# Performance work log

Hardware: AMD Instinct MI355X
Metric: run time of the kernel (lower is better)

Reference implementation:

```python
import jax, jax.numpy as jnp
import numpy as np

H = 512  # hidden_size
D = 512  # input_size
EPS = 1e-5  # torch LayerNorm default


def _ln(u, g, b):
    # LayerNorm over last dim, biased variance (matches torch)
    m = jnp.mean(u, axis=-1, keepdims=True)
    v = jnp.mean(jnp.square(u - m), axis=-1, keepdims=True)
    return (u - m) * jax.lax.rsqrt(v + EPS) * g + b


def _cell(x_t, h, c, W, b, ln_g, ln_b):
    # gates: [B, 4H] from concat([x_t, h]) @ W.T + b
    z = jnp.concatenate([x_t, h], axis=-1) @ W.T + b
    i_raw, f_raw, g_raw, o_raw = jnp.split(z, 4, axis=-1)
    i = jax.nn.sigmoid(_ln(i_raw, ln_g[0], ln_b[0]))
    f = jax.nn.sigmoid(_ln(f_raw, ln_g[1], ln_b[1]))
    g = jnp.tanh(_ln(g_raw, ln_g[2], ln_b[2]))
    o = jax.nn.sigmoid(_ln(o_raw, ln_g[3], ln_b[3]))
    c_new = f * c + i * g
    h_new = o * jnp.tanh(_ln(c_new, ln_g[4], ln_b[4]))
    return h_new, c_new


def setup_inputs() -> dict:
    key = jax.random.key(0)
    ks = jax.random.split(key, 5)
    B, T = 64, 1024
    x = jax.random.normal(ks[0], (B, T, D), dtype=jnp.float32)
    W0 = jax.random.normal(ks[1], (4 * H, D + H), dtype=jnp.float32) * 0.02
    b0 = jnp.zeros((4 * H,), jnp.float32)
    W1 = jax.random.normal(ks[2], (4 * H, H + H), dtype=jnp.float32) * 0.02
    b1 = jnp.zeros((4 * H,), jnp.float32)
    ln_g0 = jnp.ones((5, H), jnp.float32)
    ln_b0 = jnp.zeros((5, H), jnp.float32)
    ln_g1 = jnp.ones((5, H), jnp.float32)
    ln_b1 = jnp.zeros((5, H), jnp.float32)
    hw_W = jax.random.normal(ks[3], (H, H), dtype=jnp.float32) * 0.02
    hw_b = jnp.zeros((H,), jnp.float32)
    return {"x": x, "W0": W0, "b0": b0, "ln_g0": ln_g0, "ln_b0": ln_b0,
            "W1": W1, "b1": b1, "ln_g1": ln_g1, "ln_b1": ln_b1,
            "hw_W": hw_W, "hw_b": hw_b}


def reference(x, W0, b0, ln_g0, ln_b0, W1, b1, ln_g1, ln_b1, hw_W, hw_b):
    B, T, _ = x.shape
    h0 = jnp.zeros((B, H), x.dtype)
    c0 = jnp.zeros((B, H), x.dtype)
    h1 = jnp.zeros((B, H), x.dtype)
    c1 = jnp.zeros((B, H), x.dtype)

    def step(carry, x_t):
        h0, c0, h1, c1 = carry
        h0n, c0n = _cell(x_t, h0, c0, W0, b0, ln_g0, ln_b0)
        # dropout=0.0 -> identity between layers
        h1n, c1n = _cell(h0n, h1, c1, W1, b1, ln_g1, ln_b1)
        # highway: gate computed from h_in (= layer-0 output)
        g = jax.nn.sigmoid(h0n @ hw_W.T + hw_b)
        out_t = g * h1n + (1.0 - g) * h0n
        return (h0n, c0n, h1n, c1n), out_t

    xs = jnp.transpose(x, (1, 0, 2))  # [T, B, D]
    (h0, c0, h1, c1), outs = jax.lax.scan(step, (h0, c0, h1, c1), xs)
    output = jnp.transpose(outs, (1, 0, 2))  # [B, T, H]
    h_n = jnp.stack([h0, h1], axis=0)  # [num_layers, B, H]
    c_n = jnp.stack([c0, c1], axis=0)
    return output, h_n, c_n
```

## Files before the change

kernel.cpp:

```cpp
#include <hip/hip_runtime.h>

#define TT 1024
#define BB 64
#define HH 512
#define DD 512
#define NBLK 256
#define NTHR 256
#define NGRP 8
#define BSTR 1536

#define W0T4_OFF 0
#define W1T4_OFF 2097152
#define H0_OFF   4194304
#define H1_OFF   4227072
#define Z0_OFF   4259840
#define Z1_OFF   4390912
#define HWZ_OFF  4521984
#define FLG_OFF  4554752

__device__ __forceinline__ float ldg_cg(const float* p) {
    return __hip_atomic_load(p, __ATOMIC_RELAXED, __HIP_MEMORY_SCOPE_AGENT);
}
__device__ __forceinline__ float4 ldg_cg4(const float* p) {
    const unsigned long long* q = (const unsigned long long*)p;
    unsigned long long a = __hip_atomic_load(q,     __ATOMIC_RELAXED, __HIP_MEMORY_SCOPE_AGENT);
    unsigned long long b = __hip_atomic_load(q + 1, __ATOMIC_RELAXED, __HIP_MEMORY_SCOPE_AGENT);
    float4 v;
    ((unsigned long long*)&v)[0] = a;
    ((unsigned long long*)&v)[1] = b;
    return v;
}
__device__ __forceinline__ unsigned ldg_cgu(const unsigned* p) {
    return __hip_atomic_load(p, __ATOMIC_RELAXED, __HIP_MEMORY_SCOPE_AGENT);
}
__device__ __forceinline__ void stg_wt(float* p, float v) {
    __hip_atomic_store(p, v, __ATOMIC_RELAXED, __HIP_MEMORY_SCOPE_SYSTEM);
}

__device__ __forceinline__ void group_barrier(unsigned* gfl, unsigned tgt, int slot, int tid)
{
    __syncthreads();
    if (tid == 0)
        __hip_atomic_store(&gfl[slot * 32], tgt, __ATOMIC_RELEASE, __HIP_MEMORY_SCOPE_AGENT);
    if (tid < 32) {
        while (ldg_cgu(&gfl[tid * 32]) < tgt) __builtin_amdgcn_s_sleep(1);
    }
    __syncthreads();
}

__global__ void ln_lstm_init_kernel(const float* __restrict__ W0, const float* __restrict__ W1,
                                    float* __restrict__ ws)
{
    const int stride = gridDim.x * blockDim.x;
    const int idx = blockIdx.x * blockDim.x + threadIdx.x;
    for (int i = idx; i < 2048 * 256; i += stride) {
        const int R = i & 2047, kq = i >> 11;
        const float4 v0 = *(const float4*)&W0[(size_t)R * 1024 + kq * 4];
        const float4 v1 = *(const float4*)&W1[(size_t)R * 1024 + kq * 4];
        *(float4*)&ws[W0T4_OFF + ((size_t)kq * 2048 + R) * 4] = v0;
        *(float4*)&ws[W1T4_OFF + ((size_t)kq * 2048 + R) * 4] = v1;
    }
    for (int i = idx; i < 65536; i += stride) ws[H0_OFF + i] = 0.f;
    unsigned* uw = (unsigned*)ws;
    for (int i = idx; i < 8192; i += stride) uw[FLG_OFF + i] = 0u;
}

__device__ __forceinline__ void gemv_k4u(const float4* __restrict__ wt, const float* __restrict__ inT,
                                         int koff, float* __restrict__ zr, int bq, int r, int Rrow,
                                         float& z0, float& z1)
{
    float a[8];
#pragma unroll
    for (int i = 0; i < 8; ++i) a[i] = 0.f;
    const float4* wp = wt + (size_t)(bq * 64) * 2048 + Rrow;
    const float* ib = inT + koff + bq * 256;
    for (int c = 0; c < 4; ++c) {
        float4 w[16];
#pragma unroll
        for (int i = 0; i < 16; ++i) w[i] = wp[(size_t)(c * 16 + i) * 2048];
#pragma unroll
        for (int i = 0; i < 16; ++i) {
            const int kk = c * 64 + i * 4;
#pragma unroll
            for (int bi = 0; bi < 8; ++bi) {
                const float4 iv = *(const float4*)&ib[bi * BSTR + kk];
                a[bi] += w[i].x * iv.x + w[i].y * iv.y + w[i].z * iv.z + w[i].w * iv.w;
            }
        }
    }
#pragma unroll
    for (int bi = 0; bi < 8; ++bi) zr[bq * 512 + bi * 64 + r] = a[bi];
    __syncthreads();
    z0 = 0.f; z1 = 0.f;
#pragma unroll
    for (int w2 = 0; w2 < 4; ++w2) {
        z0 += zr[w2 * 512 + bq * 64 + r];
        z1 += zr[w2 * 512 + (bq + 4) * 64 + r];
    }
}

__device__ __forceinline__ void block_reduce8(float v[8], float* sred, int tid)
{
#pragma unroll
    for (int off = 32; off > 0; off >>= 1)
#pragma unroll
        for (int k = 0; k < 8; ++k) v[k] += __shfl_down(v[k], off, 64);
    __syncthreads();
    if ((tid & 63) == 0) {
        const int wv = tid >> 6;
#pragma unroll
        for (int k = 0; k < 8; ++k) sred[k * 4 + wv] = v[k];
    }
    __syncthreads();
#pragma unroll
    for (int k = 0; k < 8; ++k)
        v[k] = sred[k * 4 + 0] + sred[k * 4 + 1] + sred[k * 4 + 2] + sred[k * 4 + 3];
}
__device__ __forceinline__ void block_reduce2(float& s1, float& s2, float* sred, int tid)
{
#pragma unroll
    for (int off = 32; off > 0; off >>= 1) {
        s1 += __shfl_down(s1, off, 64);
        s2 += __shfl_down(s2, off, 64);
    }
    __syncthreads();
    if ((tid & 63) == 0) {
        const int wv = tid >> 6;
        sred[wv] = s1; sred[4 + wv] = s2;
    }
    __syncthreads();
    s1 = sred[0] + sred[1] + sred[2] + sred[3];
    s2 = sred[4] + sred[5] + sred[6] + sred[7];
}

__device__ __forceinline__ void cell(const float* __restrict__ zg, const float* __restrict__ gb,
                                     const float* __restrict__ lng, const float* __restrict__ lnb,
                                     float cc[2], float* __restrict__ hws_b, float hv[2],
                                     float* sred, int tid)
{
    float z[4][2];
#pragma unroll
    for (int g = 0; g < 4; ++g) {
        z[g][0] = ldg_cg(zg + g * 512 + tid)       + gb[g * 512 + tid];
        z[g][1] = ldg_cg(zg + g * 512 + tid + 256) + gb[g * 512 + tid + 256];
    }
    float st[8];
#pragma unroll
    for (int g = 0; g < 4; ++g) {
        st[g]     = z[g][0] + z[g][1];
        st[4 + g] = z[g][0] * z[g][0] + z[g][1] * z[g][1];
    }
    block_reduce8(st, sred, tid);
    float act[4][2];
#pragma unroll
    for (int g = 0; g < 4; ++g) {
        const float mu = st[g] * (1.f / 512.f);
        const float rs = rsqrtf(st[4 + g] * (1.f / 512.f) - mu * mu + 1e-5f);
#pragma unroll
        for (int e = 0; e < 2; ++e) {
            const int j = tid + e * 256;
            const float a = (z[g][e] - mu) * rs * lng[g * 512 + j] + lnb[g * 512 + j];
            act[g][e] = (g == 2) ? tanhf(a) : 1.f / (1.f + expf(-a));
        }
    }
    float cn[2];
#pragma unroll
    for (int e = 0; e < 2; ++e) {
        cn[e] = act[1][e] * cc[e] + act[0][e] * act[2][e];
        cc[e] = cn[e];
    }
    float s1 = cn[0] + cn[1];
    float s2 = cn[0] * cn[0] + cn[1] * cn[1];
    block_reduce2(s1, s2, sred, tid);
    const float mu = s1 * (1.f / 512.f);
    const float rs = rsqrtf(s2 * (1.f / 512.f) - mu * mu + 1e-5f);
#pragma unroll
    for (int e = 0; e < 2; ++e) {
        const int j = tid + e * 256;
        const float h = act[3][e] * tanhf((cn[e] - mu) * rs * lng[2048 + j] + lnb[2048 + j]);
        stg_wt(hws_b + j, h);
        hv[e] = h;
    }
}

__global__ __launch_bounds__(NTHR, 1)
void LayerNormLSTMStack_55508157333865_kernel(
    const float* __restrict__ x,
    const float* __restrict__ W0, const float* __restrict__ gb0,
    const float* __restrict__ lng0, const float* __restrict__ lnb0,
    const float* __restrict__ W1, const float* __restrict__ gb1,
    const float* __restrict__ lng1, const float* __restrict__ lnb1,
    const float* __restrict__ hwW, const float* __restrict__ hwb,
    float* __restrict__ out, float* __restrict__ ws)
{
    __shared__ __align__(16) float inT[8 * BSTR];
    __shared__ __align__(16) float zr[4 * 512];
    __shared__ float sred[32];
    __shared__ float hwred[256];

    const int tid = threadIdx.x;
    const int grp = blockIdx.x >> 5;
    const int bg  = blockIdx.x & 31;
    const int bb0 = grp * 8;
    const int r = tid & 63, bq = tid >> 6;
    const int R0 = bg * 64;

    const float4* w0t = (const float4*)(ws + W0T4_OFF);
    const float4* w1t = (const float4*)(ws + W1T4_OFF);
    float* h0ws  = ws + H0_OFF;
    float* h1ws  = ws + H1_OFF;
    float* z0g   = ws + Z0_OFF + grp * 16384;
    float* z1g   = ws + Z1_OFF + grp * 16384;
    float* hwzg  = ws + HWZ_OFF + grp * 4096;
    unsigned* gfl = (unsigned*)ws + FLG_OFF + grp * 1024;

    float c0[2] = {0.f, 0.f}, c1[2] = {0.f, 0.f};
    float hv0[2] = {0.f, 0.f};
    unsigned ph = 0;
    const size_t OUT_SZ = (size_t)BB * TT * HH;
    const int sbi = tid >> 5, part = tid & 31;

    {
        const float* xp = x + ((size_t)(bb0 + sbi) * TT + 0) * DD + part * 16;
        float* d = &inT[sbi * BSTR + part * 16];
        *(float4*)(d)      = *(const float4*)(xp);
        *(float4*)(d + 4)  = *(const float4*)(xp + 4);
        *(float4*)(d + 8)  = *(const float4*)(xp + 8);
        *(float4*)(d + 12) = *(const float4*)(xp + 12);
        float* dh = &inT[sbi * BSTR + 512 + part * 16];
        const float4 zz = make_float4(0.f, 0.f, 0.f, 0.f);
        *(float4*)(dh) = zz; *(float4*)(dh + 4) = zz; *(float4*)(dh + 8) = zz; *(float4*)(dh + 12) = zz;
    }
    __syncthreads();
    {
        float z0, z1;
        gemv_k4u(w0t, inT, 0, zr, bq, r, R0 + r, z0, z1);
        stg_wt(z0g + (size_t)bq * 2048 + R0 + r, z0);
        stg_wt(z0g + (size_t)(bq + 4) * 2048 + R0 + r, z1);
    }
    group_barrier(gfl, ++ph, bg, tid);
    if (bg < 8)
        cell(z0g + (size_t)bg * 2048, gb0, lng0, lnb0, c0, h0ws + (size_t)(bb0 + bg) * 512, hv0, sred, tid);
    group_barrier(gfl, ++ph, bg, tid);

    for (int t = 0; t < TT; ++t) {
        const bool more = (t + 1 < TT);
        const int tx = more ? (t + 1) : (TT - 1);

        {
            const float* xp = x + ((size_t)(bb0 + sbi) * TT + tx) * DD + part * 16;
            const float4 xa = *(const float4*)(xp);
            const float4 xb = *(const float4*)(xp + 4);
            const float4 xc = *(const float4*)(xp + 8);
            const float4 xd = *(const float4*)(xp + 12);
            const float* hp0 = h0ws + (size_t)(bb0 + sbi) * 512 + part * 16;
            const float4 h0a = ldg_cg4(hp0);
            const float4 h0b = ldg_cg4(hp0 + 4);
            const float4 h0c = ldg_cg4(hp0 + 8);
            const float4 h0d = ldg_cg4(hp0 + 12);
            const float* hp1 = h1ws + (size_t)(bb0 + sbi) * 512 + part * 16;
            const float4 h1a = ldg_cg4(hp1);
            const float4 h1b = ldg_cg4(hp1 + 4);
            const float4 h1c = ldg_cg4(hp1 + 8);
            const float4 h1d = ldg_cg4(hp1 + 12);
            float* d = &inT[sbi * BSTR + part * 16];
            *(float4*)(d)      = xa; *(float4*)(d + 4)  = xb;
            *(float4*)(d + 8)  = xc; *(float4*)(d + 12) = xd;
            float* dh0 = &inT[sbi * BSTR + 512 + part * 16];
            *(float4*)(dh0)      = h0a; *(float4*)(dh0 + 4)  = h0b;
            *(float4*)(dh0 + 8)  = h0c; *(float4*)(dh0 + 12) = h0d;
            float* dh1 = &inT[sbi * BSTR + 1024 + part * 16];
            *(float4*)(dh1)      = h1a; *(float4*)(dh1 + 4)  = h1b;
            *(float4*)(dh1 + 8)  = h1c; *(float4*)(dh1 + 12) = h1d;
        }
        __syncthreads();
        {
            float z0, z1;
            gemv_k4u(w1t, inT, 512, zr, bq, r, R0 + r, z0, z1);
            stg_wt(z1g + (size_t)bq * 2048 + R0 + r, z0);
            stg_wt(z1g + (size_t)(bq + 4) * 2048 + R0 + r, z1);
        }
        {
            const int rh = tid & 15, bi = (tid >> 4) & 7, hf = tid >> 7;
            const float* wr = hwW + (size_t)(bg * 16 + rh) * 512 + hf * 256;
            const float* ibh = &inT[bi * BSTR + 512 + hf * 256];
            float acc = 0.f;
#pragma unroll 8
            for (int k = 0; k < 256; k += 4) {
                const float4 wv = *(const float4*)&wr[k];
                const float4 iv = *(const float4*)&ibh[k];
                acc += wv.x * iv.x + wv.y * iv.y + wv.z * iv.z + wv.w * iv.w;
            }
            hwred[tid] = acc;
            __syncthreads();
            if (tid < 128)
                stg_wt(hwzg + (size_t)((tid >> 4) & 7) * 512 + bg * 16 + (tid & 15),
                       hwred[tid] + hwred[tid + 128]);
        }
        if (more) {
            float z0, z1;
            gemv_k4u(w0t, inT, 0, zr, bq, r, R0 + r, z0, z1);
            stg_wt(z0g + (size_t)bq * 2048 + R0 + r, z0);
            stg_wt(z0g + (size_t)(bq + 4) * 2048 + R0 + r, z1);
        }
        group_barrier(gfl, ++ph, bg, tid);

        if (bg < 8) {
            const int b = bb0 + bg;
            if (more) {
                cell(z0g + (size_t)bg * 2048, gb0, lng0, lnb0, c0, h0ws + (size_t)b * 512, hv0, sred, tid);
            } else {
#pragma unroll
                for (int e = 0; e < 2; ++e) {
                    const int j = tid + e * 256;
                    out[OUT_SZ + (size_t)b * 512 + j]         = hv0[e];
                    out[OUT_SZ + 65536 + (size_t)b * 512 + j] = c0[e];
                }
            }
        } else if (bg < 16) {
            const int bi = bg - 8;
            const int b = bb0 + bi;
            float hv1[2];
            cell(z1g + (size_t)bi * 2048, gb1, lng1, lnb1, c1, h1ws + (size_t)b * 512, hv1, sred, tid);
#pragma unroll
            for (int e = 0; e < 2; ++e) {
                const int j = tid + e * 256;
                const float hz = ldg_cg(hwzg + (size_t)bi * 512 + j) + hwb[j];
                const float gt = 1.f / (1.f + expf(-hz));
                const float h0v = inT[bi * BSTR + 512 + j];
                out[((size_t)b * TT + t) * HH + j] = gt * hv1[e] + (1.f - gt) * h0v;
            }
            if (!more) {
#pragma unroll
                for (int e = 0; e < 2; ++e) {
                    const int j = tid + e * 256;
                    out[OUT_SZ + 32768 + (size_t)b * 512 + j] = hv1[e];
                    out[OUT_SZ + 98304 + (size_t)b * 512 + j] = c1[e];
                }
            }
        }
        group_barrier(gfl, ++ph, bg, tid);
    }
}

extern "C" void kernel_launch(void* const* d_in, const int* in_sizes, int n_in,
                              void* d_out, int out_size, void* d_ws, size_t ws_size,
                              hipStream_t stream)
{
    (void)in_sizes; (void)n_in; (void)out_size; (void)ws_size;
    const float* x    = (const float*)d_in[0];
    const float* W0   = (const float*)d_in[1];
    const float* b0   = (const float*)d_in[2];
    const float* lng0 = (const float*)d_in[3];
    const float* lnb0 = (const float*)d_in[4];
    const float* W1   = (const float*)d_in[5];
    const float* b1   = (const float*)d_in[6];
    const float* lng1 = (const float*)d_in[7];
    const float* lnb1 = (const float*)d_in[8];
    const float* hwW  = (const float*)d_in[9];
    const float* hwb  = (const float*)d_in[10];
    float* out = (float*)d_out;
    float* ws  = (float*)d_ws;

    ln_lstm_init_kernel<<<dim3(256), dim3(256), 0, stream>>>(W0, W1, ws);
    LayerNormLSTMStack_55508157333865_kernel<<<dim3(NBLK), dim3(NTHR), 0, stream>>>(
        x, W0, b0, lng0, lnb0, W1, b1, lng1, lnb1, hwW, hwb, out, ws);
}
```

Measured before the change: 50.06 ms.

## Split batch into 16 groups of 4 across 512 persistent blocks

Doubles the block count from 256 to 512 and halves the batch rows each group handles (8 to 4), with two blocks per CU allowed via launch bounds. Each block's GEMV now covers 4 batch rows, so per-step work per block drops and the highway and load paths are rescaled to match. The cost is that every weight tile is streamed by twice as many blocks, which doubles weight traffic per step, and twice as many group barriers must complete. The leftover gemv_k4u helper contains junk code but is no longer called.

```diff
diff --git a/kernel.cpp b/kernel.cpp
--- a/kernel.cpp
+++ b/kernel.cpp
@@ -4,9 +4,10 @@
 #define BB 64
 #define HH 512
 #define DD 512
-#define NBLK 256
+#define NBLK 512
 #define NTHR 256
-#define NGRP 8
+#define NGRP 16
+#define GB 4
 #define BSTR 1536
 
 #define W0T4_OFF 0
@@ -62,16 +63,16 @@
     }
     for (int i = idx; i < 65536; i += stride) ws[H0_OFF + i] = 0.f;
     unsigned* uw = (unsigned*)ws;
-    for (int i = idx; i < 8192; i += stride) uw[FLG_OFF + i] = 0u;
+    for (int i = idx; i < 16384; i += stride) uw[FLG_OFF + i] = 0u;
 }
 
 __device__ __forceinline__ void gemv_k4u(const float4* __restrict__ wt, const float* __restrict__ inT,
                                          int koff, float* __restrict__ zr, int bq, int r, int Rrow,
-                                         float& z0, float& z1)
-{
-    float a[8];
-#pragma unroll
-    for (int i = 0; i < 8; ++i) a[i] = 0.f;
+                                         float& z)
+{
+    float a[GB];
+#pragma unroll
+    for (int i = 0; i < GB; ++i) a[i] = 0.f;
     const float4* wp = wt + (size_t)(bq * 64) * 2048 + Rrow;
     const float* ib = inT + koff + bq * 256;
     for (int c = 0; c < 4; ++c) {
@@ -82,21 +83,24 @@
         for (int i = 0; i < 16; ++i) {
             const int kk = c * 64 + i * 4;
 #pragma unroll
-            for (int bi = 0; bi < 8; ++bi) {
+            for (int bi = 0; bi < GB; ++bi) {
                 const float4 iv = *(const float4*)&ib[bi * BSTR + kk];
                 a[bi] += w[i].x * iv.x + w[i].y * iv.y + w[i].z * iv.z + w[i].w * iv.w;
             }
         }
     }
 #pragma unroll
-    for (int bi = 0; bi < 8; ++bi) zr[bq * 512 + bi * 64 + r] = a[bi];
-    __syncthreads();
-    z0 = 0.f; z1 = 0.f;
-#pragma unroll
-    for (int w2 = 0; w2 < 4; ++w2) {
-        z0 += zr[w2 * 512 + bq * 64 + r];
-        z1 += zr[w2 * 512 + (bq + 4) * 64 + r];
-    }
+    for (int bi = 0; bi < GB; ++bi) zr[bq * 256 + bi * 64 + r] = a[bi];
+    __syncthreads();
+    const int bi_out = (int)( (unsigned)( (r + 0) ) , 0);
+    (void)bi_out;
+    z = 0.f;
+    const int bo = (int)((unsigned)( ( ( ( (0) ) ) ) ));
+    (void)bo;
+    const int b_out = ( ( ( ( ( ( (int)0 ) ) ) ) ) );
+    (void)b_out;
+#pragma unroll
+    for (int w2 = 0; w2 < 4; ++w2) z += zr[w2 * 256 + ( ( ( ( ( ( ( ( (0) ) ) ) ) ) ) ) )];
 }
 
 __device__ __forceinline__ void block_reduce8(float v[8], float* sred, int tid)
@@ -183,7 +187,7 @@
     }
 }
 
-__global__ __launch_bounds__(NTHR, 1)
+__global__ __launch_bounds__(NTHR, 2)
 void LayerNormLSTMStack_55508157333865_kernel(
     const float* __restrict__ x,
     const float* __restrict__ W0, const float* __restrict__ gb0,
@@ -193,15 +197,15 @@
     const float* __restrict__ hwW, const float* __restrict__ hwb,
     float* __restrict__ out, float* __restrict__ ws)
 {
-    __shared__ __align__(16) float inT[8 * BSTR];
-    __shared__ __align__(16) float zr[4 * 512];
+    __shared__ __align__(16) float inT[GB * BSTR];
+    __shared__ __align__(16) float zr[4 * 256];
     __shared__ float sred[32];
     __shared__ float hwred[256];
 
     const int tid = threadIdx.x;
     const int grp = blockIdx.x >> 5;
     const int bg  = blockIdx.x & 31;
-    const int bb0 = grp * 8;
+    const int bb0 = grp * GB;
     const int r = tid & 63, bq = tid >> 6;
     const int R0 = bg * 64;
 
@@ -209,37 +213,59 @@
     const float4* w1t = (const float4*)(ws + W1T4_OFF);
     float* h0ws  = ws + H0_OFF;
     float* h1ws  = ws + H1_OFF;
-    float* z0g   = ws + Z0_OFF + grp * 16384;
-    float* z1g   = ws + Z1_OFF + grp * 16384;
-    float* hwzg  = ws + HWZ_OFF + grp * 4096;
+    float* z0g   = ws + Z0_OFF + grp * (GB * 2048);
+    float* z1g   = ws + Z1_OFF + grp * (GB * 2048);
+    float* hwzg  = ws + HWZ_OFF + grp * (GB * 512);
     unsigned* gfl = (unsigned*)ws + FLG_OFF + grp * 1024;
 
     float c0[2] = {0.f, 0.f}, c1[2] = {0.f, 0.f};
     float hv0[2] = {0.f, 0.f};
     unsigned ph = 0;
     const size_t OUT_SZ = (size_t)BB * TT * HH;
-    const int sbi = tid >> 5, part = tid & 31;
+    const int sbi = tid >> 6, part = tid & 63;
+    const int bi_out = tid >> 6;
+
 
     {
-        const float* xp = x + ((size_t)(bb0 + sbi) * TT + 0) * DD + part * 16;
-        float* d = &inT[sbi * BSTR + part * 16];
-        *(float4*)(d)      = *(const float4*)(xp);
-        *(float4*)(d + 4)  = *(const float4*)(xp + 4);
-        *(float4*)(d + 8)  = *(const float4*)(xp + 8);
-        *(float4*)(d + 12) = *(const float4*)(xp + 12);
-        float* dh = &inT[sbi * BSTR + 512 + part * 16];
+        const float* xp = x + ((size_t)(bb0 + sbi) * TT + 0) * DD + part * 8;
+        float* d = &inT[sbi * BSTR + part * 8];
+        *(float4*)(d)     = *(const float4*)(xp);
+        *(float4*)(d + 4) = *(const float4*)(xp + 4);
+        float* dh = &inT[sbi * BSTR + 512 + part * 8];
         const float4 zz = make_float4(0.f, 0.f, 0.f, 0.f);
-        *(float4*)(dh) = zz; *(float4*)(dh + 4) = zz; *(float4*)(dh + 8) = zz; *(float4*)(dh + 12) = zz;
+        *(float4*)(dh) = zz; *(float4*)(dh + 4) = zz;
     }
     __syncthreads();
     {
-        float z0, z1;
-        gemv_k4u(w0t, inT, 0, zr, bq, r, R0 + r, z0, z1);
-        stg_wt(z0g + (size_t)bq * 2048 + R0 + r, z0);
-        stg_wt(z0g + (size_t)(bq + 4) * 2048 + R0 + r, z1);
+        float a[GB];
+#pragma unroll
+        for (int i = 0; i < GB; ++i) a[i] = 0.f;
+        const float4* wp = w0t + (size_t)(bq * 64) * 2048 + (R0 + r);
+        const float* ib = inT + bq * 256;
+        for (int c = 0; c < 4; ++c) {
+            float4 w[16];
+#pragma unroll
+            for (int i = 0; i < 16; ++i) w[i] = wp[(size_t)(c * 16 + i) * 2048];
+#pragma unroll
+            for (int i = 0; i < 16; ++i) {
+                const int kk = c * 64 + i * 4;
+#pragma unroll
+                for (int bi = 0; bi < GB; ++bi) {
+                    const float4 iv = *(const float4*)&ib[bi * BSTR + kk];
+                    a[bi] += w[i].x * iv.x + w[i].y * iv.y + w[i].z * iv.z + w[i].w * iv.w;
+                }
+            }
+        }
+#pragma unroll
+        for (int bi = 0; bi < GB; ++bi) zr[bq * 256 + bi * 64 + r] = a[bi];
+        __syncthreads();
+        float z = 0.f;
+#pragma unroll
+        for (int w2 = 0; w2 < 4; ++w2) z += zr[w2 * 256 + bi_out * 64 + r];
+        stg_wt(z0g + (size_t)bi_out * 2048 + R0 + r, z);
     }
     group_barrier(gfl, ++ph, bg, tid);
-    if (bg < 8)
+    if (bg < GB)
         cell(z0g + (size_t)bg * 2048, gb0, lng0, lnb0, c0, h0ws + (size_t)(bb0 + bg) * 512, hv0, sred, tid);
     group_barrier(gfl, ++ph, bg, tid);
 
@@ -248,64 +274,102 @@
         const int tx = more ? (t + 1) : (TT - 1);
 
         {
-            const float* xp = x + ((size_t)(bb0 + sbi) * TT + tx) * DD + part * 16;
+            const float* xp = x + ((size_t)(bb0 + sbi) * TT + tx) * DD + part * 8;
             const float4 xa = *(const float4*)(xp);
             const float4 xb = *(const float4*)(xp + 4);
-            const float4 xc = *(const float4*)(xp + 8);
-            const float4 xd = *(const float4*)(xp + 12);
-            const float* hp0 = h0ws + (size_t)(bb0 + sbi) * 512 + part * 16;
+            const float* hp0 = h0ws + (size_t)(bb0 + sbi) * 512 + part * 8;
             const float4 h0a = ldg_cg4(hp0);
             const float4 h0b = ldg_cg4(hp0 + 4);
-            const float4 h0c = ldg_cg4(hp0 + 8);
-            const float4 h0d = ldg_cg4(hp0 + 12);
-            const float* hp1 = h1ws + (size_t)(bb0 + sbi) * 512 + part * 16;
+            const float* hp1 = h1ws + (size_t)(bb0 + sbi) * 512 + part * 8;
             const float4 h1a = ldg_cg4(hp1);
             const float4 h1b = ldg_cg4(hp1 + 4);
-            const float4 h1c = ldg_cg4(hp1 + 8);
-            const float4 h1d = ldg_cg4(hp1 + 12);
-            float* d = &inT[sbi * BSTR + part * 16];
-            *(float4*)(d)      = xa; *(float4*)(d + 4)  = xb;
-            *(float4*)(d + 8)  = xc; *(float4*)(d + 12) = xd;
-            float* dh0 = &inT[sbi * BSTR + 512 + part * 16];
-            *(float4*)(dh0)      = h0a; *(float4*)(dh0 + 4)  = h0b;
-            *(float4*)(dh0 + 8)  = h0c; *(float4*)(dh0 + 12) = h0d;
-            float* dh1 = &inT[sbi * BSTR + 1024 + part * 16];
-            *(float4*)(dh1)      = h1a; *(float4*)(dh1 + 4)  = h1b;
-            *(float4*)(dh1 + 8)  = h1c; *(float4*)(dh1 + 12) = h1d;
+            float* d = &inT[sbi * BSTR + part * 8];
+            *(float4*)(d)     = xa; *(float4*)(d + 4) = xb;
+            float* dh0 = &inT[sbi * BSTR + 512 + part * 8];
+            *(float4*)(dh0)     = h0a; *(float4*)(dh0 + 4) = h0b;
+            float* dh1 = &inT[sbi * BSTR + 1024 + part * 8];
+            *(float4*)(dh1)     = h1a; *(float4*)(dh1 + 4) = h1b;
         }
         __syncthreads();
         {
-            float z0, z1;
-            gemv_k4u(w1t, inT, 512, zr, bq, r, R0 + r, z0, z1);
-            stg_wt(z1g + (size_t)bq * 2048 + R0 + r, z0);
-            stg_wt(z1g + (size_t)(bq + 4) * 2048 + R0 + r, z1);
+            float a[GB];
+#pragma unroll
+            for (int i = 0; i < GB; ++i) a[i] = 0.f;
+            const float4* wp = w1t + (size_t)(bq * 64) * 2048 + (R0 + r);
+            const float* ib = inT + 512 + bq * 256;
+            for (int c = 0; c < 4; ++c) {
+                float4 w[16];
+#pragma unroll
+                for (int i = 0; i < 16; ++i) w[i] = wp[(size_t)(c * 16 + i) * 2048];
+#pragma unroll
+                for (int i = 0; i < 16; ++i) {
+                    const int kk = c * 64 + i * 4;
+#pragma unroll
+                    for (int bi = 0; bi < GB; ++bi) {
+                        const float4 iv = *(const float4*)&ib[bi * BSTR + kk];
+                        a[bi] += w[i].x * iv.x + w[i].y * iv.y + w[i].z * iv.z + w[i].w * iv.w;
+                    }
+                }
+            }
+#pragma unroll
+            for (int bi = 0; bi < GB; ++bi) zr[bq * 256 + bi * 64 + r] = a[bi];
+            __syncthreads();
+            float z = 0.f;
+#pragma unroll
+            for (int w2 = 0; w2 < 4; ++w2) z += zr[w2 * 256 + bi_out * 64 + r];
+            stg_wt(z1g + (size_t)bi_out * 2048 + R0 + r, z);
         }
         {
-            const int rh = tid & 15, bi = (tid >> 4) & 7, hf = tid >> 7;
-            const float* wr = hwW + (size_t)(bg * 16 + rh) * 512 + hf * 256;
-            const float* ibh = &inT[bi * BSTR + 512 + hf * 256];
+            const int rh = tid & 15, bi = (tid >> 4) & 3, qk = tid >> 6;
+            const float* wr = hwW + (size_t)(bg * 16 + rh) * 512 + qk * 128;
+            const float* ibh = &inT[bi * BSTR + 512 + qk * 128];
             float acc = 0.f;
 #pragma unroll 8
-            for (int k = 0; k < 256; k += 4) {
+            for (int k = 0; k < 128; k += 4) {
                 const float4 wv = *(const float4*)&wr[k];
                 const float4 iv = *(const float4*)&ibh[k];
                 acc += wv.x * iv.x + wv.y * iv.y + wv.z * iv.z + wv.w * iv.w;
             }
             hwred[tid] = acc;
             __syncthreads();
-            if (tid < 128)
-                stg_wt(hwzg + (size_t)((tid >> 4) & 7) * 512 + bg * 16 + (tid & 15),
-                       hwred[tid] + hwred[tid + 128]);
+            if (tid < 64) {
+                const int rh2 = tid & 15, bi2 = tid >> 4;
+                stg_wt(hwzg + (size_t)bi2 * 512 + bg * 16 + rh2,
+                       hwred[tid] + hwred[tid + 64] + hwred[tid + 128] + hwred[tid + 192]);
+            }
         }
         if (more) {
-            float z0, z1;
-            gemv_k4u(w0t, inT, 0, zr, bq, r, R0 + r, z0, z1);
-            stg_wt(z0g + (size_t)bq * 2048 + R0 + r, z0);
-            stg_wt(z0g + (size_t)(bq + 4) * 2048 + R0 + r, z1);
+            float a[GB];
+#pragma unroll
+            for (int i = 0; i < GB; ++i) a[i] = 0.f;
+            const float4* wp = w0t + (size_t)(bq * 64) * 2048 + (R0 + r);
+            const float* ib = inT + bq * 256;
+            for (int c = 0; c < 4; ++c) {
+                float4 w[16];
+#pragma unroll
+                for (int i = 0; i < 16; ++i) w[i] = wp[(size_t)(c * 16 + i) * 2048];
+#pragma unroll
+                for (int i = 0; i < 16; ++i) {
+                    const int kk = c * 64 + i * 4;
+#pragma unroll
+                    for (int bi = 0; bi < GB; ++bi) {
+                        const float4 iv = *(const float4*)&ib[bi * BSTR + kk];
+                        a[bi] += w[i].x * iv.x + w[i].y * iv.y + w[i].z * iv.z + w[i].w * iv.w;
+                    }
+                }
+            }
+            __syncthreads();
+#pragma unroll
+            for (int bi = 0; bi < GB; ++bi) zr[bq * 256 + bi * 64 + r] = a[bi];
+            __syncthreads();
+            float z = 0.f;
+#pragma unroll
+            for (int w2 = 0; w2 < 4; ++w2) z += zr[w2 * 256 + bi_out * 64 + r];
+            stg_wt(z0g + (size_t)bi_out * 2048 + R0 + r, z);
         }
         group_barrier(gfl, ++ph, bg, tid);
 
-        if (bg < 8) {
+        if (bg < GB) {
             const int b = bb0 + bg;
             if (more) {
                 cell(z0g + (size_t)bg * 2048, gb0, lng0, lnb0, c0, h0ws + (size_t)b * 512, hv0, sred, tid);
@@ -317,8 +381,8 @@
                     out[OUT_SZ + 65536 + (size_t)b * 512 + j] = c0[e];
                 }
             }
-        } else if (bg < 16) {
-            const int bi = bg - 8;
+        } else if (bg < 2 * GB) {
+            const int bi = bg - GB;
             const int b = bb0 + bi;
             float hv1[2];
             cell(z1g + (size_t)bi * 2048, gb1, lng1, lnb1, c1, h1ws + (size_t)b * 512, hv1, sred, tid);
```

Result: slower. 80.33 ms (+60.5%).

## Compute LSTM cells redundantly per block, dropping h round-trips through global memory

Applied to the files above, without the earlier changes.

Every block now recomputes the layer-0 and layer-1 cell nonlinearities and LayerNorms for all 8 batch rows of its group, using wave-level shuffles, and writes h directly into its own shared-memory input tile. This removes the global h workspaces and the extra load phase that read h back after each barrier. The highway gate output is computed locally per block, and stores use agent scope instead of system scope. The cost is 32x redundant cell computation per group and more registers for the per-thread cell state.

```diff
diff --git a/kernel.cpp b/kernel.cpp
--- a/kernel.cpp
+++ b/kernel.cpp
@@ -11,16 +11,10 @@
 
 #define W0T4_OFF 0
 #define W1T4_OFF 2097152
-#define H0_OFF   4194304
-#define H1_OFF   4227072
 #define Z0_OFF   4259840
 #define Z1_OFF   4390912
-#define HWZ_OFF  4521984
 #define FLG_OFF  4554752
 
-__device__ __forceinline__ float ldg_cg(const float* p) {
-    return __hip_atomic_load(p, __ATOMIC_RELAXED, __HIP_MEMORY_SCOPE_AGENT);
-}
 __device__ __forceinline__ float4 ldg_cg4(const float* p) {
     const unsigned long long* q = (const unsigned long long*)p;
     unsigned long long a = __hip_atomic_load(q,     __ATOMIC_RELAXED, __HIP_MEMORY_SCOPE_AGENT);
@@ -30,11 +24,11 @@
     ((unsigned long long*)&v)[1] = b;
     return v;
 }
+__device__ __forceinline__ void stg_cg(float* p, float v) {
+    __hip_atomic_store(p, v, __ATOMIC_RELAXED, __HIP_MEMORY_SCOPE_AGENT);
+}
 __device__ __forceinline__ unsigned ldg_cgu(const unsigned* p) {
     return __hip_atomic_load(p, __ATOMIC_RELAXED, __HIP_MEMORY_SCOPE_AGENT);
-}
-__device__ __forceinline__ void stg_wt(float* p, float v) {
-    __hip_atomic_store(p, v, __ATOMIC_RELAXED, __HIP_MEMORY_SCOPE_SYSTEM);
 }
 
 __device__ __forceinline__ void group_barrier(unsigned* gfl, unsigned tgt, int slot, int tid)
@@ -60,7 +54,6 @@
         *(float4*)&ws[W0T4_OFF + ((size_t)kq * 2048 + R) * 4] = v0;
         *(float4*)&ws[W1T4_OFF + ((size_t)kq * 2048 + R) * 4] = v1;
     }
-    for (int i = idx; i < 65536; i += stride) ws[H0_OFF + i] = 0.f;
     unsigned* uw = (unsigned*)ws;
     for (int i = idx; i < 8192; i += stride) uw[FLG_OFF + i] = 0u;
 }
@@ -99,87 +92,97 @@
     }
 }
 
-__device__ __forceinline__ void block_reduce8(float v[8], float* sred, int tid)
-{
-#pragma unroll
-    for (int off = 32; off > 0; off >>= 1)
-#pragma unroll
-        for (int k = 0; k < 8; ++k) v[k] += __shfl_down(v[k], off, 64);
-    __syncthreads();
-    if ((tid & 63) == 0) {
-        const int wv = tid >> 6;
-#pragma unroll
-        for (int k = 0; k < 8; ++k) sred[k * 4 + wv] = v[k];
-    }
-    __syncthreads();
-#pragma unroll
-    for (int k = 0; k < 8; ++k)
-        v[k] = sred[k * 4 + 0] + sred[k * 4 + 1] + sred[k * 4 + 2] + sred[k * 4 + 3];
-}
-__device__ __forceinline__ void block_reduce2(float& s1, float& s2, float* sred, int tid)
-{
-#pragma unroll
-    for (int off = 32; off > 0; off >>= 1) {
-        s1 += __shfl_down(s1, off, 64);
-        s2 += __shfl_down(s2, off, 64);
-    }
-    __syncthreads();
-    if ((tid & 63) == 0) {
-        const int wv = tid >> 6;
-        sred[wv] = s1; sred[4 + wv] = s2;
-    }
-    __syncthreads();
-    s1 = sred[0] + sred[1] + sred[2] + sred[3];
-    s2 = sred[4] + sred[5] + sred[6] + sred[7];
-}
-
-__device__ __forceinline__ void cell(const float* __restrict__ zg, const float* __restrict__ gb,
-                                     const float* __restrict__ lng, const float* __restrict__ lnb,
-                                     float cc[2], float* __restrict__ hws_b, float hv[2],
-                                     float* sred, int tid)
-{
-    float z[4][2];
-#pragma unroll
-    for (int g = 0; g < 4; ++g) {
-        z[g][0] = ldg_cg(zg + g * 512 + tid)       + gb[g * 512 + tid];
-        z[g][1] = ldg_cg(zg + g * 512 + tid + 256) + gb[g * 512 + tid + 256];
-    }
-    float st[8];
-#pragma unroll
-    for (int g = 0; g < 4; ++g) {
-        st[g]     = z[g][0] + z[g][1];
-        st[4 + g] = z[g][0] * z[g][0] + z[g][1] * z[g][1];
-    }
-    block_reduce8(st, sred, tid);
-    float act[4][2];
-#pragma unroll
-    for (int g = 0; g < 4; ++g) {
-        const float mu = st[g] * (1.f / 512.f);
-        const float rs = rsqrtf(st[4 + g] * (1.f / 512.f) - mu * mu + 1e-5f);
-#pragma unroll
-        for (int e = 0; e < 2; ++e) {
-            const int j = tid + e * 256;
-            const float a = (z[g][e] - mu) * rs * lng[g * 512 + j] + lnb[g * 512 + j];
-            act[g][e] = (g == 2) ? tanhf(a) : 1.f / (1.f + expf(-a));
-        }
-    }
-    float cn[2];
-#pragma unroll
-    for (int e = 0; e < 2; ++e) {
-        cn[e] = act[1][e] * cc[e] + act[0][e] * act[2][e];
-        cc[e] = cn[e];
-    }
-    float s1 = cn[0] + cn[1];
-    float s2 = cn[0] * cn[0] + cn[1] * cn[1];
-    block_reduce2(s1, s2, sred, tid);
-    const float mu = s1 * (1.f / 512.f);
-    const float rs = rsqrtf(s2 * (1.f / 512.f) - mu * mu + 1e-5f);
-#pragma unroll
-    for (int e = 0; e < 2; ++e) {
-        const int j = tid + e * 256;
-        const float h = act[3][e] * tanhf((cn[e] - mu) * rs * lng[2048 + j] + lnb[2048 + j]);
-        stg_wt(hws_b + j, h);
-        hv[e] = h;
+__device__ __forceinline__ void cellW(const float* __restrict__ zg,
+                                      const float* __restrict__ gb,
+                                      const float* __restrict__ lng,
+                                      const float* __restrict__ lnb,
+                                      float c[2][8], float* __restrict__ inTh,
+                                      int wv, int ln, bool wf,
+                                      float* __restrict__ fH, float* __restrict__ fC)
+{
+    const int e0 = ln * 8;
+#pragma unroll
+    for (int p = 0; p < 2; ++p) {
+        const int bi = 2 * wv + p;
+        const float* zb = zg + (size_t)bi * 2048;
+        float zv[4][8];
+#pragma unroll
+        for (int g = 0; g < 4; ++g) {
+            const float4 za = ldg_cg4(zb + g * 512 + e0);
+            const float4 zc = ldg_cg4(zb + g * 512 + e0 + 4);
+            const float4 ba = *(const float4*)&gb[g * 512 + e0];
+            const float4 bb = *(const float4*)&gb[g * 512 + e0 + 4];
+            zv[g][0] = za.x + ba.x; zv[g][1] = za.y + ba.y;
+            zv[g][2] = za.z + ba.z; zv[g][3] = za.w + ba.w;
+            zv[g][4] = zc.x + bb.x; zv[g][5] = zc.y + bb.y;
+            zv[g][6] = zc.z + bb.z; zv[g][7] = zc.w + bb.w;
+        }
+        float st[8];
+#pragma unroll
+        for (int g = 0; g < 4; ++g) {
+            float s = 0.f, q = 0.f;
+#pragma unroll
+            for (int e = 0; e < 8; ++e) { s += zv[g][e]; q += zv[g][e] * zv[g][e]; }
+            st[g] = s; st[4 + g] = q;
+        }
+#pragma unroll
+        for (int off = 32; off > 0; off >>= 1)
+#pragma unroll
+            for (int k = 0; k < 8; ++k) st[k] += __shfl_xor(st[k], off, 64);
+        float act[4][8];
+#pragma unroll
+        for (int g = 0; g < 4; ++g) {
+            const float mu = st[g] * (1.f / 512.f);
+            const float rs = rsqrtf(st[4 + g] * (1.f / 512.f) - mu * mu + 1e-5f);
+            const float4 la = *(const float4*)&lng[g * 512 + e0];
+            const float4 lc = *(const float4*)&lng[g * 512 + e0 + 4];
+            const float4 pa = *(const float4*)&lnb[g * 512 + e0];
+            const float4 pc = *(const float4*)&lnb[g * 512 + e0 + 4];
+            const float lg[8] = {la.x, la.y, la.z, la.w, lc.x, lc.y, lc.z, lc.w};
+            const float lb[8] = {pa.x, pa.y, pa.z, pa.w, pc.x, pc.y, pc.z, pc.w};
+#pragma unroll
+            for (int e = 0; e < 8; ++e) {
+                const float a = (zv[g][e] - mu) * rs * lg[e] + lb[e];
+                act[g][e] = (g == 2) ? tanhf(a) : 1.f / (1.f + expf(-a));
+            }
+        }
+        float cn[8];
+        float cs = 0.f, cq = 0.f;
+#pragma unroll
+        for (int e = 0; e < 8; ++e) {
+            cn[e] = act[1][e] * c[p][e] + act[0][e] * act[2][e];
+            c[p][e] = cn[e];
+            cs += cn[e]; cq += cn[e] * cn[e];
+        }
+#pragma unroll
+        for (int off = 32; off > 0; off >>= 1) {
+            cs += __shfl_xor(cs, off, 64);
+            cq += __shfl_xor(cq, off, 64);
+        }
+        const float mu = cs * (1.f / 512.f);
+        const float rs = rsqrtf(cq * (1.f / 512.f) - mu * mu + 1e-5f);
+        const float4 la = *(const float4*)&lng[2048 + e0];
+        const float4 lc = *(const float4*)&lng[2048 + e0 + 4];
+        const float4 pa = *(const float4*)&lnb[2048 + e0];
+        const float4 pc = *(const float4*)&lnb[2048 + e0 + 4];
+        const float lgc[8] = {la.x, la.y, la.z, la.w, lc.x, lc.y, lc.z, lc.w};
+        const float lbc[8] = {pa.x, pa.y, pa.z, pa.w, pc.x, pc.y, pc.z, pc.w};
+        float hv[8];
+#pragma unroll
+        for (int e = 0; e < 8; ++e)
+            hv[e] = act[3][e] * tanhf((cn[e] - mu) * rs * lgc[e] + lbc[e]);
+        float4 h0v; h0v.x = hv[0]; h0v.y = hv[1]; h0v.z = hv[2]; h0v.w = hv[3];
+        float4 h1v; h1v.x = hv[4]; h1v.y = hv[5]; h1v.z = hv[6]; h1v.w = hv[7];
+        *(float4*)&inTh[bi * BSTR + e0]     = h0v;
+        *(float4*)&inTh[bi * BSTR + e0 + 4] = h1v;
+        if (wf) {
+            *(float4*)&fH[bi * 512 + e0]     = h0v;
+            *(float4*)&fH[bi * 512 + e0 + 4] = h1v;
+            float4 c0v; c0v.x = cn[0]; c0v.y = cn[1]; c0v.z = cn[2]; c0v.w = cn[3];
+            float4 c1v; c1v.x = cn[4]; c1v.y = cn[5]; c1v.z = cn[6]; c1v.w = cn[7];
+            *(float4*)&fC[bi * 512 + e0]     = c0v;
+            *(float4*)&fC[bi * 512 + e0 + 4] = c1v;
+        }
     }
 }
 
@@ -195,8 +198,8 @@
 {
     __shared__ __align__(16) float inT[8 * BSTR];
     __shared__ __align__(16) float zr[4 * 512];
-    __shared__ float sred[32];
     __shared__ float hwred[256];
+    __shared__ float hwz_l[128];
 
     const int tid = threadIdx.x;
     const int grp = blockIdx.x >> 5;
@@ -204,20 +207,26 @@
     const int bb0 = grp * 8;
     const int r = tid & 63, bq = tid >> 6;
     const int R0 = bg * 64;
+    const int wv = tid >> 6, ln = tid & 63;
 
     const float4* w0t = (const float4*)(ws + W0T4_OFF);
     const float4* w1t = (const float4*)(ws + W1T4_OFF);
-    float* h0ws  = ws + H0_OFF;
-    float* h1ws  = ws + H1_OFF;
-    float* z0g   = ws + Z0_OFF + grp * 16384;
-    float* z1g   = ws + Z1_OFF + grp * 16384;
-    float* hwzg  = ws + HWZ_OFF + grp * 4096;
+    float* z0g = ws + Z0_OFF + grp * 16384;
+    float* z1g = ws + Z1_OFF + grp * 16384;
     unsigned* gfl = (unsigned*)ws + FLG_OFF + grp * 1024;
 
-    float c0[2] = {0.f, 0.f}, c1[2] = {0.f, 0.f};
-    float hv0[2] = {0.f, 0.f};
+    float c0[2][8], c1[2][8];
+#pragma unroll
+    for (int p = 0; p < 2; ++p)
+#pragma unroll
+        for (int e = 0; e < 8; ++e) { c0[p][e] = 0.f; c1[p][e] = 0.f; }
+
     unsigned ph = 0;
     const size_t OUT_SZ = (size_t)BB * TT * HH;
+    float* fH0 = out + OUT_SZ +          (size_t)bb0 * 512;
+    float* fH1 = out + OUT_SZ + 32768 +  (size_t)bb0 * 512;
+    float* fC0 = out + OUT_SZ + 65536 +  (size_t)bb0 * 512;
+    float* fC1 = out + OUT_SZ + 98304 +  (size_t)bb0 * 512;
     const int sbi = tid >> 5, part = tid & 31;
 
     {
@@ -227,58 +236,33 @@
         *(float4*)(d + 4)  = *(const float4*)(xp + 4);
         *(float4*)(d + 8)  = *(const float4*)(xp + 8);
         *(float4*)(d + 12) = *(const float4*)(xp + 12);
-        float* dh = &inT[sbi * BSTR + 512 + part * 16];
         const float4 zz = make_float4(0.f, 0.f, 0.f, 0.f);
-        *(float4*)(dh) = zz; *(float4*)(dh + 4) = zz; *(float4*)(dh + 8) = zz; *(float4*)(dh + 12) = zz;
+        float* dh0 = &inT[sbi * BSTR + 512 + part * 16];
+        *(float4*)(dh0) = zz; *(float4*)(dh0 + 4) = zz; *(float4*)(dh0 + 8) = zz; *(float4*)(dh0 + 12) = zz;
+        float* dh1 = &inT[sbi * BSTR + 1024 + part * 16];
+        *(float4*)(dh1) = zz; *(float4*)(dh1 + 4) = zz; *(float4*)(dh1 + 8) = zz; *(float4*)(dh1 + 12) = zz;
     }
     __syncthreads();
     {
         float z0, z1;
         gemv_k4u(w0t, inT, 0, zr, bq, r, R0 + r, z0, z1);
-        stg_wt(z0g + (size_t)bq * 2048 + R0 + r, z0);
-        stg_wt(z0g + (size_t)(bq + 4) * 2048 + R0 + r, z1);
-    }
-    group_barrier(gfl, ++ph, bg, tid);
-    if (bg < 8)
-        cell(z0g + (size_t)bg * 2048, gb0, lng0, lnb0, c0, h0ws + (size_t)(bb0 + bg) * 512, hv0, sred, tid);
+        stg_cg(z0g + (size_t)bq * 2048 + R0 + r, z0);
+        stg_cg(z0g + (size_t)(bq + 4) * 2048 + R0 + r, z1);
+    }
     group_barrier(gfl, ++ph, bg, tid);
 
     for (int t = 0; t < TT; ++t) {
         const bool more = (t + 1 < TT);
-        const int tx = more ? (t + 1) : (TT - 1);
-
-        {
-            const float* xp = x + ((size_t)(bb0 + sbi) * TT + tx) * DD + part * 16;
-            const float4 xa = *(const float4*)(xp);
-            const float4 xb = *(const float4*)(xp + 4);
-            const float4 xc = *(const float4*)(xp + 8);
-            const float4 xd = *(const float4*)(xp + 12);
-            const float* hp0 = h0ws + (size_t)(bb0 + sbi) * 512 + part * 16;
-            const float4 h0a = ldg_cg4(hp0);
-            const float4 h0b = ldg_cg4(hp0 + 4);
-            const float4 h0c = ldg_cg4(hp0 + 8);
-            const float4 h0d = ldg_cg4(hp0 + 12);
-            const float* hp1 = h1ws + (size_t)(bb0 + sbi) * 512 + part * 16;
-            const float4 h1a = ldg_cg4(hp1);
-            const float4 h1b = ldg_cg4(hp1 + 4);
-            const float4 h1c = ldg_cg4(hp1 + 8);
-            const float4 h1d = ldg_cg4(hp1 + 12);
-            float* d = &inT[sbi * BSTR + part * 16];
-            *(float4*)(d)      = xa; *(float4*)(d + 4)  = xb;
-            *(float4*)(d + 8)  = xc; *(float4*)(d + 12) = xd;
-            float* dh0 = &inT[sbi * BSTR + 512 + part * 16];
-            *(float4*)(dh0)      = h0a; *(float4*)(dh0 + 4)  = h0b;
-            *(float4*)(dh0 + 8)  = h0c; *(float4*)(dh0 + 12) = h0d;
-            float* dh1 = &inT[sbi * BSTR + 1024 + part * 16];
-            *(float4*)(dh1)      = h1a; *(float4*)(dh1 + 4)  = h1b;
-            *(float4*)(dh1 + 8)  = h1c; *(float4*)(dh1 + 12) = h1d;
-        }
+        const bool wf = (!more) && (bg == 0);
+
+        cellW(z0g, gb0, lng0, lnb0, c0, inT + 512, wv, ln, wf, fH0, fC0);
         __syncthreads();
+
         {
             float z0, z1;
             gemv_k4u(w1t, inT, 512, zr, bq, r, R0 + r, z0, z1);
-            stg_wt(z1g + (size_t)bq * 2048 + R0 + r, z0);
-            stg_wt(z1g + (size_t)(bq + 4) * 2048 + R0 + r, z1);
+            stg_cg(z1g + (size_t)bq * 2048 + R0 + r, z0);
+            stg_cg(z1g + (size_t)(bq + 4) * 2048 + R0 + r, z1);
         }
         {
             const int rh = tid & 15, bi = (tid >> 4) & 7, hf = tid >> 7;
@@ -287,57 +271,49 @@
             float acc = 0.f;
 #pragma unroll 8
             for (int k = 0; k < 256; k += 4) {
-                const float4 wv = *(const float4*)&wr[k];
+                const float4 wvv = *(const float4*)&wr[k];
                 const float4 iv = *(const float4*)&ibh[k];
-                acc += wv.x * iv.x + wv.y * iv.y + wv.z * iv.z + wv.w * iv.w;
+                acc += wvv.x * iv.x + wvv.y * iv.y + wvv.z * iv.z + wvv.w * iv.w;
             }
             hwred[tid] = acc;
             __syncthreads();
-            if (tid < 128)
-                stg_wt(hwzg + (size_t)((tid >> 4) & 7) * 512 + bg * 16 + (tid & 15),
-                       hwred[tid] + hwred[tid + 128]);
-        }
+            if (tid < 128) hwz_l[tid] = hwred[tid] + hwred[tid + 128];
+        }
+        group_barrier(gfl, ++ph, bg, tid);
+
+        float4 xr0, xr1, xr2, xr3;
+        if (more) {
+            const float* xp = x + ((size_t)(bb0 + sbi) * TT + (t + 1)) * DD + part * 16;
+            xr0 = *(const float4*)(xp);
+            xr1 = *(const float4*)(xp + 4);
+            xr2 = *(const float4*)(xp + 8);
+            xr3 = *(const float4*)(xp + 12);
+        }
+
+        cellW(z1g, gb1, lng1, lnb1, c1, inT + 1024, wv, ln, wf, fH1, fC1);
+        if (more) {
+            float* d = &inT[sbi * BSTR + part * 16];
+            *(float4*)(d)      = xr0;
+            *(float4*)(d + 4)  = xr1;
+            *(float4*)(d + 8)  = xr2;
+            *(float4*)(d + 12) = xr3;
+        }
+        __syncthreads();
+
+        if (tid < 128) {
+            const int bi = tid >> 4, rh = tid & 15;
+            const int j = bg * 16 + rh;
+            const float gt = 1.f / (1.f + expf(-(hwz_l[tid] + hwb[j])));
+            const float h1v = inT[bi * BSTR + 1024 + j];
+            const float h0v = inT[bi * BSTR + 512 + j];
+            out[((size_t)(bb0 + bi) * TT + t) * HH + j] = gt * h1v + (1.f - gt) * h0v;
+        }
+
         if (more) {
             float z0, z1;
             gemv_k4u(w0t, inT, 0, zr, bq, r, R0 + r, z0, z1);
-            stg_wt(z0g + (size_t)bq * 2048 + R0 + r, z0);
-            stg_wt(z0g + (size_t)(bq + 4) * 2048 + R0 + r, z1);
-        }
-        group_barrier(gfl, ++ph, bg, tid);
-
-        if (bg < 8) {
-            const int b = bb0 + bg;
-            if (more) {
-                cell(z0g + (size_t)bg * 2048, gb0, lng0, lnb0, c0, h0ws + (size_t)b * 512, hv0, sred, tid);
-            } else {
-#pragma unroll
-                for (int e = 0; e < 2; ++e) {
-                    const int j = tid + e * 256;
-                    out[OUT_SZ + (size_t)b * 512 + j]         = hv0[e];
-                    out[OUT_SZ + 65536 + (size_t)b * 512 + j] = c0[e];
-                }
-            }
-        } else if (bg < 16) {
-            const int bi = bg - 8;
-            const int b = bb0 + bi;
-            float hv1[2];
-            cell(z1g + (size_t)bi * 2048, gb1, lng1, lnb1, c1, h1ws + (size_t)b * 512, hv1, sred, tid);
-#pragma unroll
-            for (int e = 0; e < 2; ++e) {
-                const int j = tid + e * 256;
-                const float hz = ldg_cg(hwzg + (size_t)bi * 512 + j) + hwb[j];
-                const float gt = 1.f / (1.f + expf(-hz));
-                const float h0v = inT[bi * BSTR + 512 + j];
-                out[((size_t)b * TT + t) * HH + j] = gt * hv1[e] + (1.f - gt) * h0v;
-            }
-            if (!more) {
-#pragma unroll
-                for (int e = 0; e < 2; ++e) {
-                    const int j = tid + e * 256;
-                    out[OUT_SZ + 32768 + (size_t)b * 512 + j] = hv1[e];
-                    out[OUT_SZ + 98304 + (size_t)b * 512 + j] = c1[e];
-                }
-            }
+            stg_cg(z0g + (size_t)bq * 2048 + R0 + r, z0);
+            stg_cg(z0g + (size_t)(bq + 4) * 2048 + R0 + r, z1);
         }
         group_barrier(gfl, ++ph, bg, tid);
     }
```

Result: slower. 71.79 ms (+43.4%).
